# Kernel optimization log

Hardware: AMD Instinct MI355X
Metric: run time of the kernel (lower is better)

## Reference

```python
import jax, jax.numpy as jnp
import numpy as np

B_SZ, SEQ = 16, 2048
VOCAB, EMBED = 50257, 128
DSTATE, HID, NCLS = 16, 256, 10
NEDGE = 8192  # edges per graph (avg degree 4)
LN_EPS = 1e-5


def setup_inputs() -> dict:
    key = jax.random.key(0)
    ks = jax.random.split(key, 12)
    tokens = jax.random.randint(ks[0], (B_SZ, SEQ), 0, VOCAB, dtype=jnp.int32)
    lengths = jnp.full((B_SZ,), SEQ, dtype=jnp.int32)  # full-length graphs
    edge_indices = jax.random.randint(ks[1], (B_SZ, 2, NEDGE), 0, SEQ, dtype=jnp.int32)
    emb = (jax.random.normal(ks[2], (VOCAB, EMBED)) * 0.02).at[0].set(0.0)  # padding_idx=0
    A_log = jax.random.normal(ks[3], (EMBED, DSTATE)) * 0.1
    B_w = jax.random.normal(ks[4], (DSTATE, EMBED)) * (1.0 / np.sqrt(EMBED))
    C_w = jax.random.normal(ks[5], (EMBED, DSTATE)) * (1.0 / np.sqrt(DSTATE))
    D_skip = jnp.ones((EMBED,))
    ln_g = jnp.ones((EMBED,))
    ln_b = jnp.zeros((EMBED,))
    Wmsg_w = jax.random.normal(ks[6], (HID, EMBED)) * (1.0 / np.sqrt(EMBED))
    Wupd_w = jax.random.normal(ks[7], (HID, EMBED + HID)) * (1.0 / np.sqrt(EMBED + HID))
    Wupd_b = jax.random.normal(ks[8], (HID,)) * 0.01
    cls_w = jax.random.normal(ks[9], (NCLS, HID)) * (1.0 / np.sqrt(HID))
    cls_b = jnp.zeros((NCLS,))
    return {"tokens": tokens, "lengths": lengths, "edge_indices": edge_indices,
            "emb": emb, "A_log": A_log, "B_w": B_w, "C_w": C_w, "D_skip": D_skip,
            "ln_g": ln_g, "ln_b": ln_b, "Wmsg_w": Wmsg_w, "Wupd_w": Wupd_w,
            "Wupd_b": Wupd_b, "cls_w": cls_w, "cls_b": cls_b}


def _ssm(x, A_log, B_w, C_w, D_skip, ln_g, ln_b):
    # x: (B, S, d_model). Diagonal SSM: h_t = h_{t-1}*exp(A) + B x_t (broadcast over d_model)
    Aexp = jnp.exp(-jnp.exp(A_log))  # (d_model, d_state)
    h0 = jnp.zeros((x.shape[0], EMBED, DSTATE), dtype=x.dtype)

    def step(h, x_t):  # x_t: (B, d_model)
        b_t = x_t @ B_w.T                            # (B, d_state)
        h = h * Aexp[None] + b_t[:, None, :]          # (B, d_model, d_state)
        y = h.mean(axis=1) @ C_w.T + D_skip * x_t     # (B, d_model)
        return h, y

    _, ys = jax.lax.scan(step, h0, jnp.swapaxes(x, 0, 1))
    out = jnp.swapaxes(ys, 0, 1)                      # (B, S, d_model)
    mu = out.mean(-1, keepdims=True)
    var = jnp.mean((out - mu) ** 2, axis=-1, keepdims=True)
    return ln_g * (out - mu) * jax.lax.rsqrt(var + LN_EPS) + ln_b


def reference(tokens, lengths, edge_indices, emb, A_log, B_w, C_w, D_skip,
              ln_g, ln_b, Wmsg_w, Wupd_w, Wupd_b, cls_w, cls_b):
    x = emb[tokens]                                   # (B, S, E)
    h = _ssm(x, A_log, B_w, C_w, D_skip, ln_g, ln_b)  # (B, S, E)
    src, dst = edge_indices[:, 0, :], edge_indices[:, 1, :]   # (B, Ne)
    h_src = jnp.take_along_axis(h, src[:, :, None], axis=1)   # (B, Ne, E)
    msgs = jnp.einsum('bed,hd->beh', h_src, Wmsg_w)            # (B, Ne, H)
    flat_dst = (jnp.arange(B_SZ, dtype=dst.dtype)[:, None] * SEQ + dst).reshape(-1)
    agg = jax.ops.segment_sum(msgs.reshape(-1, HID), flat_dst,
                              num_segments=B_SZ * SEQ).reshape(B_SZ, SEQ, HID)
    upd = jax.nn.relu(jnp.concatenate([h, agg], axis=-1) @ Wupd_w.T + Wupd_b)  # (B, S, H)
    pooled = upd.mean(axis=1)                          # (B, H)  (all lengths == SEQ)
    return pooled @ cls_w.T + cls_b                    # (B, NCLS)
```

## Files before the change

kernel.cpp:

```cpp
#include <hip/hip_runtime.h>

#define B_SZ   16
#define SEQ    2048
#define VOCAB  50257
#define EMBED  128
#define DSTATE 16
#define HID    256
#define NCLS   10
#define NEDGE  8192
#define KTR    64
#define LN_EPS 1e-5f
#define NROW   (B_SZ*SEQ)
#define BCAP   32
#define OVCAP  1024

#define PB_BUCKET 512
#define PB_PRECM  (PB_BUCKET + 128)
#define PB_CTAB   (PB_PRECM + 16)
#define PB_TOTAL  (PB_CTAB + 1)

typedef float  f32x4 __attribute__((ext_vector_type(4)));
typedef short  s16x8 __attribute__((ext_vector_type(8)));

__device__ __forceinline__ float scrub(float x){
  return (x == x && fabsf(x) < 1e30f) ? x : 0.f;
}
__device__ __forceinline__ short f2b(float f){
  unsigned int u = __float_as_uint(f);
  unsigned int r = (u + 0x7fffu + ((u >> 16) & 1u)) >> 16;
  return (short)r;
}
__device__ __forceinline__ unsigned int pack2(float a, float b){
  return (unsigned int)(unsigned short)f2b(a)
       | ((unsigned int)(unsigned short)f2b(b) << 16);
}
__device__ __forceinline__ float lo2f(unsigned int v){ return __uint_as_float(v << 16); }
__device__ __forceinline__ float hi2f(unsigned int v){ return __uint_as_float(v & 0xffff0000u); }

__global__ __launch_bounds__(256) void k_prep(
    const float* __restrict__ A_log, const float* __restrict__ B_w,
    const float* __restrict__ Wmsg, const float* __restrict__ Wupd,
    const int* __restrict__ edges,
    float* __restrict__ c_tab, short* __restrict__ Bf, float* __restrict__ MT,
    int* __restrict__ cnt, unsigned short* __restrict__ bucket,
    int* __restrict__ ovf_cnt, int* __restrict__ ovf){
  int bid = blockIdx.x, tid = threadIdx.x;
  if (bid < PB_BUCKET){
    int eid = bid*256 + tid;
    int b = eid >> 13, i = eid & (NEDGE-1);
    const int* ei = edges + (size_t)b*2*NEDGE;
    int s = ei[i]         & (SEQ-1);
    int d = ei[NEDGE + i] & (SEQ-1);
    int gdst = (b << 11) | d;
    int slot = atomicAdd(&cnt[gdst], 1);
    if (slot < BCAP) bucket[(size_t)gdst*BCAP + slot] = (unsigned short)s;
    else {
      int o = atomicAdd(ovf_cnt, 1);
      if (o < OVCAP) ovf[o] = ((b << 11) | s) | (gdst << 16);
    }
  } else if (bid < PB_PRECM){
    int hp = (bid-PB_BUCKET)*2 + (tid >> 7);
    int e  = tid & 127;
    const float* w2 = Wupd + (size_t)hp*384 + 128;
    float acc = 0.f;
    for (int h1 = 0; h1 < HID; ++h1)
      acc += Wmsg[h1*EMBED + e] * w2[h1];
    MT[(size_t)hp*EMBED + e] = scrub(acc);
  } else if (bid < PB_CTAB){
    if (tid < 64){
      int d = bid - PB_PRECM, lane = tid;
      float a0 = scrub(expf(-expf(A_log[(2*lane+0)*DSTATE + d])));
      float a1 = scrub(expf(-expf(A_log[(2*lane+1)*DSTATE + d])));
      float p0 = 1.f, p1 = 1.f;
      for (int k = 0; k < KTR; ++k){
        float s = p0 + p1;
        for (int off = 32; off; off >>= 1) s += __shfl_down(s, off);
        if (lane == 0) c_tab[k*DSTATE + d] = scrub(s * (1.0f/128.0f));
        p0 *= a0; p1 *= a1;
      }
    }
  } else {
    int idx = tid;
    int c = idx >> 6, lane = idx & 63;
    int n = lane & 15;
    int kb = c*32 + (lane >> 4)*8;
    short v[8];
    #pragma unroll
    for (int jj = 0; jj < 8; ++jj) v[jj] = f2b(B_w[(size_t)n*EMBED + kb + jj]);
    *(s16x8*)(Bf + (size_t)idx*8) = *(s16x8*)v;
  }
}

__global__ __launch_bounds__(256) void k_ssm_fused(
    const int* __restrict__ tokens, const float* __restrict__ emb,
    const float* __restrict__ c_tab,
    const float* __restrict__ C_w, const float* __restrict__ D_skip,
    const float* __restrict__ ln_g, const float* __restrict__ ln_b,
    const short* __restrict__ Bf, const float* __restrict__ Wupd,
    const float* __restrict__ MT, unsigned int* __restrict__ h_out,
    short* __restrict__ Wcs){
  __shared__ unsigned int xsh[128][68];
  __shared__ float bsh[128][18];
  __shared__ float msh[64][18];
  __shared__ float Ct[DSTATE][EMBED+2];
  __shared__ float csh[KTR][DSTATE];
  int bid = blockIdx.x, tid = threadIdx.x;

  if (bid >= 512){
    int idx = (bid-512)*256 + tid;
    int c    = idx >> 10;
    int rem  = idx & 1023;
    int j    = rem >> 6;
    int lane = rem & 63;
    int n  = j*16 + (lane & 15);
    int kb = c*32 + (lane >> 4)*8;
    short v[8];
    #pragma unroll
    for (int jj = 0; jj < 8; ++jj){
      int k = kb + jj;
      float val = (k < 128) ? Wupd[(size_t)n*384 + k] : MT[(size_t)n*EMBED + (k-128)];
      v[jj] = f2b(val);
    }
    *(s16x8*)(Wcs + (size_t)idx*8) = *(s16x8*)v;
    return;
  }

  int b  = bid >> 5;
  int t0 = (bid & 31) * 64;

  {
    const int* tkb = tokens + b*SEQ;
    for (int i = 0; i < 16; ++i){
      int gid = i*256 + tid;
      int lr = gid >> 5, ch = gid & 31;
      int t = t0 - 64 + lr;
      uint2 o; o.x = 0u; o.y = 0u;
      if (t >= 0){
        int tok = tkb[t];
        tok = tok < 0 ? 0 : (tok >= VOCAB ? VOCAB-1 : tok);
        float4 v = *(const float4*)(emb + (size_t)tok*EMBED + ch*4);
        o.x = pack2(v.x, v.y); o.y = pack2(v.z, v.w);
      }
      *(uint2*)&xsh[lr][ch*2] = o;
    }
  }
  for (int i = tid; i < DSTATE*EMBED; i += 256){
    int e = i >> 4, d = i & 15;
    Ct[d][e] = C_w[i];
  }
  for (int i = tid; i < KTR*DSTATE; i += 256)
    csh[i >> 4][i & 15] = c_tab[i];
  __syncthreads();

  int wv = tid >> 6, lane = tid & 63;
  int m = lane & 15, lg = lane >> 4;

  const s16x8* Bp = (const s16x8*)Bf;
  #pragma unroll
  for (int tt = 0; tt < 2; ++tt){
    int tile = wv*2 + tt;
    int trow = t0 - 64 + tile*16;
    f32x4 acc = (f32x4){0.f,0.f,0.f,0.f};
    if (trow >= 0){
      const short* xrow = (const short*)&xsh[tile*16 + m][0] + lg*8;
      #pragma unroll
      for (int c = 0; c < 4; ++c){
        s16x8 a = *(const s16x8*)(xrow + c*32);
        acc = __builtin_amdgcn_mfma_f32_16x16x32_bf16(a, Bp[c*64 + lane], acc, 0, 0, 0);
      }
    }
    #pragma unroll
    for (int r = 0; r < 4; ++r)
      bsh[tile*16 + lg*4 + r][m] = scrub(acc[r]);
  }
  __syncthreads();

  {
    int d = tid & 15;
    #pragma unroll
    for (int it = 0; it < 4; ++it){
      int q = (tid + it*256) >> 4;
      int t = t0 + q;
      int base = 64 + q;
      int kmax = (t+1 < KTR) ? t+1 : KTR;
      float acc = 0.f;
      for (int k = 0; k < kmax; ++k) acc += csh[k][d] * bsh[base-k][d];
      msh[q][d] = scrub(acc);
    }
  }
  __syncthreads();

  int e0 = lane*2;
  float2 dsk = *(const float2*)&D_skip[e0];
  float2 lgv = *(const float2*)&ln_g[e0];
  float2 lbv = *(const float2*)&ln_b[e0];
  for (int q = wv*16; q < wv*16+16; ++q){
    int row = b*SEQ + t0 + q;
    unsigned int xp = xsh[64 + q][lane];
    float x0 = lo2f(xp), x1 = hi2f(xp);
    float y0 = dsk.x*x0, y1 = dsk.y*x1;
    #pragma unroll
    for (int d = 0; d < DSTATE; ++d){
      float md = msh[q][d];
      y0 += md * Ct[d][e0];
      y1 += md * Ct[d][e0+1];
    }
    y0 = scrub(y0); y1 = scrub(y1);
    float s = y0+y1, s2 = y0*y0 + y1*y1;
    for (int off = 32; off; off >>= 1){ s += __shfl_down(s,off); s2 += __shfl_down(s2,off); }
    s = __shfl(s, 0); s2 = __shfl(s2, 0);
    float mu  = s * (1.f/EMBED);
    float var = s2 * (1.f/EMBED) - mu*mu;
    float inv = rsqrtf(fmaxf(var, 0.f) + LN_EPS);
    float o0 = scrub(lgv.x*(y0-mu)*inv + lbv.x);
    float o1 = scrub(lgv.y*(y1-mu)*inv + lbv.y);
    h_out[(size_t)row*(EMBED/2) + lane] = pack2(o0, o1);
  }
}

__global__ __launch_bounds__(256) void k_gupd(
    const short* __restrict__ h, const int* __restrict__ cnt,
    const unsigned short* __restrict__ bucket,
    const int* __restrict__ ovf_cnt, const int* __restrict__ ovf,
    const short* __restrict__ Wcs, const float* __restrict__ Wupd_b,
    const float* __restrict__ cls_w, const float* __restrict__ cls_b,
    float* __restrict__ out){
  __shared__ unsigned int gsh[16][68];
  __shared__ float psum[HID];
  __shared__ float oacc[4][NCLS];
  int tid = threadIdx.x;
  int wv = tid >> 6, lane = tid & 63;
  int row0 = blockIdx.x * 16;
  int b = row0 >> 11;
  int m = lane & 15, lg = lane >> 4;

  const unsigned int* hb  = (const unsigned int*)h + (size_t)b*SEQ*(EMBED/2);
  const unsigned int* h32 = (const unsigned int*)h;
  int on = *ovf_cnt; on = on > OVCAP ? OVCAP : on;
  for (int i = 0; i < 4; ++i){
    int rloc = wv*4 + i;
    int r = row0 + rloc;
    int n = cnt[r]; n = n > BCAP ? BCAP : n;
    const unsigned short* bk = bucket + (size_t)r*BCAP;
    float ax = 0.f, ay = 0.f;
    int t = 0;
    for (; t + 4 <= n; t += 4){
      ushort4 s4 = *(const ushort4*)(bk + t);
      unsigned int v0 = hb[(size_t)s4.x*(EMBED/2) + lane];
      unsigned int v1 = hb[(size_t)s4.y*(EMBED/2) + lane];
      unsigned int v2 = hb[(size_t)s4.z*(EMBED/2) + lane];
      unsigned int v3 = hb[(size_t)s4.w*(EMBED/2) + lane];
      ax += lo2f(v0); ay += hi2f(v0);
      ax += lo2f(v1); ay += hi2f(v1);
      ax += lo2f(v2); ay += hi2f(v2);
      ax += lo2f(v3); ay += hi2f(v3);
    }
    for (; t < n; ++t){
      unsigned int v = hb[(size_t)bk[t]*(EMBED/2) + lane];
      ax += lo2f(v); ay += hi2f(v);
    }
    for (int idx = 0; idx < on; ++idx){
      int pk = ovf[idx];
      if (((pk >> 16) & 0x7fff) == r){
        unsigned int v = h32[(size_t)(pk & 0xffff)*(EMBED/2) + lane];
        ax += lo2f(v); ay += hi2f(v);
      }
    }
    gsh[rloc][lane] = pack2(scrub(ax), scrub(ay));
  }
  __syncthreads();

  const short* hrow = h + (size_t)(row0+m)*EMBED + lg*8;
  s16x8 hfrag[4], gfrag[4];
  #pragma unroll
  for (int c = 0; c < 4; ++c){
    hfrag[c] = *(const s16x8*)(hrow + c*32);
    gfrag[c] = *(const s16x8*)&gsh[m][c*16 + lg*4];
  }

  int j0 = wv*4;
  f32x4 acc[4];
  #pragma unroll
  for (int jj = 0; jj < 4; ++jj) acc[jj] = (f32x4){0.f,0.f,0.f,0.f};
  const s16x8* Bp = (const s16x8*)Wcs;
  #pragma unroll
  for (int c = 0; c < 8; ++c){
    s16x8 a = (c < 4) ? hfrag[c] : gfrag[c-4];
    #pragma unroll
    for (int jj = 0; jj < 4; ++jj){
      s16x8 bfr = Bp[(c*16 + j0 + jj)*64 + lane];
      acc[jj] = __builtin_amdgcn_mfma_f32_16x16x32_bf16(a, bfr, acc[jj], 0, 0, 0);
    }
  }

  #pragma unroll
  for (int jj = 0; jj < 4; ++jj){
    int n = (j0 + jj)*16 + m;
    float bias = Wupd_b[n];
    float v = 0.f;
    #pragma unroll
    for (int r = 0; r < 4; ++r) v += fmaxf(acc[jj][r] + bias, 0.f);
    v += __shfl_down(v, 32);
    v += __shfl_down(v, 16);
    if (lane < 16) psum[n] = scrub(v);
  }
  __syncthreads();

  {
    float pn = psum[tid];
    #pragma unroll
    for (int c = 0; c < NCLS; ++c){
      float t = pn * cls_w[c*HID + tid];
      for (int off = 32; off; off >>= 1) t += __shfl_down(t, off);
      if (lane == 0) oacc[wv][c] = t;
    }
    __syncthreads();
    if (tid < NCLS){
      float s = oacc[0][tid] + oacc[1][tid] + oacc[2][tid] + oacc[3][tid];
      atomicAdd(&out[b*NCLS + tid], scrub(s * (1.0f/SEQ)));
    }
    if ((blockIdx.x & 127) == 0 && tid < NCLS)
      atomicAdd(&out[b*NCLS + tid], cls_b[tid]);
  }
}

extern "C" void kernel_launch(void* const* d_in, const int* in_sizes, int n_in,
                              void* d_out, int out_size, void* d_ws, size_t ws_size,
                              hipStream_t stream) {
  const int*   tokens = (const int*)d_in[0];
  const int*   edges  = (const int*)d_in[2];
  const float* emb    = (const float*)d_in[3];
  const float* A_log  = (const float*)d_in[4];
  const float* B_w    = (const float*)d_in[5];
  const float* C_w    = (const float*)d_in[6];
  const float* D_skip = (const float*)d_in[7];
  const float* ln_g   = (const float*)d_in[8];
  const float* ln_b   = (const float*)d_in[9];
  const float* Wmsg   = (const float*)d_in[10];
  const float* Wupd   = (const float*)d_in[11];
  const float* Wupd_b = (const float*)d_in[12];
  const float* cls_w  = (const float*)d_in[13];
  const float* cls_b  = (const float*)d_in[14];
  float* out = (float*)d_out;

  char* ws = (char*)d_ws;
  float* c_tab = (float*)ws;  ws += 16*1024;
  float* MT    = (float*)ws;  ws += (size_t)HID*EMBED*4;
  short* Wcs   = (short*)ws;  ws += (size_t)HID*HID*2;
  short* Bf    = (short*)ws;  ws += 16*1024;
  char*  zbase = ws;
  int*   cnt   = (int*)ws;    ws += (size_t)NROW*4;
  int*   ovf_cnt = (int*)ws;  ws += 64;
  int*   ovf   = (int*)ws;    ws += OVCAP*4;
  size_t zlen = (size_t)((char*)ws - zbase);
  unsigned short* bucket = (unsigned short*)ws; ws += (size_t)NROW*BCAP*2;
  short* h_bf  = (short*)ws;  ws += (size_t)NROW*EMBED*2;

  hipMemsetAsync(zbase, 0, zlen, stream);
  hipMemsetAsync(out, 0, (size_t)B_SZ*NCLS*4, stream);
  hipLaunchKernelGGL(k_prep, dim3(PB_TOTAL), dim3(256), 0, stream,
                     A_log, B_w, Wmsg, Wupd, edges,
                     c_tab, Bf, MT, cnt, bucket, ovf_cnt, ovf);
  hipLaunchKernelGGL(k_ssm_fused, dim3(544), dim3(256), 0, stream,
                     tokens, emb, c_tab, C_w, D_skip, ln_g, ln_b, Bf, Wupd, MT,
                     (unsigned int*)h_bf, Wcs);
  hipLaunchKernelGGL(k_gupd, dim3(NROW/16), dim3(256), 0, stream,
                     h_bf, cnt, bucket, ovf_cnt, ovf, Wcs, Wupd_b,
                     cls_w, cls_b, out);
}
```

Measured before the change: 180.1 us.

## Move edge bucketing into SSM kernel and widen gather loads to uint2

```diff
diff --git a/kernel.cpp b/kernel.cpp
--- a/kernel.cpp
+++ b/kernel.cpp
@@ -14,8 +14,7 @@
 #define BCAP   32
 #define OVCAP  1024
 
-#define PB_BUCKET 512
-#define PB_PRECM  (PB_BUCKET + 128)
+#define PB_PRECM  128
 #define PB_CTAB   (PB_PRECM + 16)
 #define PB_TOTAL  (PB_CTAB + 1)
 
@@ -40,26 +39,10 @@
 __global__ __launch_bounds__(256) void k_prep(
     const float* __restrict__ A_log, const float* __restrict__ B_w,
     const float* __restrict__ Wmsg, const float* __restrict__ Wupd,
-    const int* __restrict__ edges,
-    float* __restrict__ c_tab, short* __restrict__ Bf, float* __restrict__ MT,
-    int* __restrict__ cnt, unsigned short* __restrict__ bucket,
-    int* __restrict__ ovf_cnt, int* __restrict__ ovf){
+    float* __restrict__ c_tab, short* __restrict__ Bf, float* __restrict__ MT){
   int bid = blockIdx.x, tid = threadIdx.x;
-  if (bid < PB_BUCKET){
-    int eid = bid*256 + tid;
-    int b = eid >> 13, i = eid & (NEDGE-1);
-    const int* ei = edges + (size_t)b*2*NEDGE;
-    int s = ei[i]         & (SEQ-1);
-    int d = ei[NEDGE + i] & (SEQ-1);
-    int gdst = (b << 11) | d;
-    int slot = atomicAdd(&cnt[gdst], 1);
-    if (slot < BCAP) bucket[(size_t)gdst*BCAP + slot] = (unsigned short)s;
-    else {
-      int o = atomicAdd(ovf_cnt, 1);
-      if (o < OVCAP) ovf[o] = ((b << 11) | s) | (gdst << 16);
-    }
-  } else if (bid < PB_PRECM){
-    int hp = (bid-PB_BUCKET)*2 + (tid >> 7);
+  if (bid < PB_PRECM){
+    int hp = bid*2 + (tid >> 7);
     int e  = tid & 127;
     const float* w2 = Wupd + (size_t)hp*384 + 128;
     float acc = 0.f;
@@ -98,13 +81,31 @@
     const float* __restrict__ ln_g, const float* __restrict__ ln_b,
     const short* __restrict__ Bf, const float* __restrict__ Wupd,
     const float* __restrict__ MT, unsigned int* __restrict__ h_out,
-    short* __restrict__ Wcs){
+    short* __restrict__ Wcs, const int* __restrict__ edges,
+    int* __restrict__ cnt, unsigned short* __restrict__ bucket,
+    int* __restrict__ ovf_cnt, int* __restrict__ ovf){
   __shared__ unsigned int xsh[128][68];
   __shared__ float bsh[128][18];
   __shared__ float msh[64][18];
   __shared__ float Ct[DSTATE][EMBED+2];
   __shared__ float csh[KTR][DSTATE];
   int bid = blockIdx.x, tid = threadIdx.x;
+
+  if (bid >= 544){
+    int eid = (bid-544)*256 + tid;
+    int b2 = eid >> 13, i = eid & (NEDGE-1);
+    const int* ei = edges + (size_t)b2*2*NEDGE;
+    int s = ei[i]         & (SEQ-1);
+    int d = ei[NEDGE + i] & (SEQ-1);
+    int gdst = (b2 << 11) | d;
+    int slot = atomicAdd(&cnt[gdst], 1);
+    if (slot < BCAP) bucket[(size_t)gdst*BCAP + slot] = (unsigned short)s;
+    else {
+      int o = atomicAdd(ovf_cnt, 1);
+      if (o < OVCAP) ovf[o] = ((b2 << 11) | s) | (gdst << 16);
+    }
+    return;
+  }
 
   if (bid >= 512){
     int idx = (bid-512)*256 + tid;
@@ -237,36 +238,40 @@
   const unsigned int* hb  = (const unsigned int*)h + (size_t)b*SEQ*(EMBED/2);
   const unsigned int* h32 = (const unsigned int*)h;
   int on = *ovf_cnt; on = on > OVCAP ? OVCAP : on;
-  for (int i = 0; i < 4; ++i){
-    int rloc = wv*4 + i;
+  int hh = lane >> 5;
+  int lw = lane & 31;
+  for (int i = 0; i < 2; ++i){
+    int rloc = wv*4 + i*2 + hh;
     int r = row0 + rloc;
     int n = cnt[r]; n = n > BCAP ? BCAP : n;
     const unsigned short* bk = bucket + (size_t)r*BCAP;
-    float ax = 0.f, ay = 0.f;
+    float ax0=0.f, ay0=0.f, ax1=0.f, ay1=0.f;
     int t = 0;
     for (; t + 4 <= n; t += 4){
       ushort4 s4 = *(const ushort4*)(bk + t);
-      unsigned int v0 = hb[(size_t)s4.x*(EMBED/2) + lane];
-      unsigned int v1 = hb[(size_t)s4.y*(EMBED/2) + lane];
-      unsigned int v2 = hb[(size_t)s4.z*(EMBED/2) + lane];
-      unsigned int v3 = hb[(size_t)s4.w*(EMBED/2) + lane];
-      ax += lo2f(v0); ay += hi2f(v0);
-      ax += lo2f(v1); ay += hi2f(v1);
-      ax += lo2f(v2); ay += hi2f(v2);
-      ax += lo2f(v3); ay += hi2f(v3);
+      uint2 v0 = *(const uint2*)&hb[(size_t)s4.x*(EMBED/2) + lw*2];
+      uint2 v1 = *(const uint2*)&hb[(size_t)s4.y*(EMBED/2) + lw*2];
+      uint2 v2 = *(const uint2*)&hb[(size_t)s4.z*(EMBED/2) + lw*2];
+      uint2 v3 = *(const uint2*)&hb[(size_t)s4.w*(EMBED/2) + lw*2];
+      ax0 += lo2f(v0.x); ay0 += hi2f(v0.x); ax1 += lo2f(v0.y); ay1 += hi2f(v0.y);
+      ax0 += lo2f(v1.x); ay0 += hi2f(v1.x); ax1 += lo2f(v1.y); ay1 += hi2f(v1.y);
+      ax0 += lo2f(v2.x); ay0 += hi2f(v2.x); ax1 += lo2f(v2.y); ay1 += hi2f(v2.y);
+      ax0 += lo2f(v3.x); ay0 += hi2f(v3.x); ax1 += lo2f(v3.y); ay1 += hi2f(v3.y);
     }
     for (; t < n; ++t){
-      unsigned int v = hb[(size_t)bk[t]*(EMBED/2) + lane];
-      ax += lo2f(v); ay += hi2f(v);
+      uint2 v = *(const uint2*)&hb[(size_t)bk[t]*(EMBED/2) + lw*2];
+      ax0 += lo2f(v.x); ay0 += hi2f(v.x); ax1 += lo2f(v.y); ay1 += hi2f(v.y);
     }
     for (int idx = 0; idx < on; ++idx){
       int pk = ovf[idx];
       if (((pk >> 16) & 0x7fff) == r){
-        unsigned int v = h32[(size_t)(pk & 0xffff)*(EMBED/2) + lane];
-        ax += lo2f(v); ay += hi2f(v);
+        uint2 v = *(const uint2*)&h32[(size_t)(pk & 0xffff)*(EMBED/2) + lw*2];
+        ax0 += lo2f(v.x); ay0 += hi2f(v.x); ax1 += lo2f(v.y); ay1 += hi2f(v.y);
       }
     }
-    gsh[rloc][lane] = pack2(scrub(ax), scrub(ay));
+    uint2 o; o.x = pack2(scrub(ax0), scrub(ay0));
+    o.y = pack2(scrub(ax1), scrub(ay1));
+    *(uint2*)&gsh[rloc][lw*2] = o;
   }
   __syncthreads();
 
@@ -359,11 +364,10 @@
   hipMemsetAsync(zbase, 0, zlen, stream);
   hipMemsetAsync(out, 0, (size_t)B_SZ*NCLS*4, stream);
   hipLaunchKernelGGL(k_prep, dim3(PB_TOTAL), dim3(256), 0, stream,
-                     A_log, B_w, Wmsg, Wupd, edges,
-                     c_tab, Bf, MT, cnt, bucket, ovf_cnt, ovf);
-  hipLaunchKernelGGL(k_ssm_fused, dim3(544), dim3(256), 0, stream,
+                     A_log, B_w, Wmsg, Wupd, c_tab, Bf, MT);
+  hipLaunchKernelGGL(k_ssm_fused, dim3(1056), dim3(256), 0, stream,
                      tokens, emb, c_tab, C_w, D_skip, ln_g, ln_b, Bf, Wupd, MT,
-                     (unsigned int*)h_bf, Wcs);
+                     (unsigned int*)h_bf, Wcs, edges, cnt, bucket, ovf_cnt, ovf);
   hipLaunchKernelGGL(k_gupd, dim3(NROW/16), dim3(256), 0, stream,
                      h_bf, cnt, bucket, ovf_cnt, ovf, Wcs, Wupd_b,
                      cls_w, cls_b, out);
```

New measurement: 179.9 us. Within noise of the previous version (-0.1%).
